# Performance work log

Hardware: AMD Instinct MI355X
Metric: run time of the kernel (lower is better)

Reference implementation:

```python
import jax, jax.numpy as jnp
import numpy as np

EPS = 1e-6
SIGMA_C = 2.0
PAD = 0
VOCAB = 100
D_EMB = 384


def setup_inputs() -> dict:
    key = jax.random.key(0)
    k1, k2, k3 = jax.random.split(key, 3)
    B, L = 32, 1025  # L odd so durs[:,1::2] and durs[:,2::2] align
    text = jax.random.randint(k1, (B, L), 0, VOCAB)
    durs = jax.random.randint(k2, (B, L), 0, 4)
    emb_table = jax.random.normal(k3, (VOCAB, D_EMB), dtype=jnp.float32)
    return {"text": text, "durs": durs, "emb_table": emb_table, "total_time": 2048}


def reference(text, durs, emb_table, total_time):
    # --- merge blank/token pairs (as in GaussianEmbedding.forward) ---
    text_m = jnp.concatenate([text[:, :1], text[:, 1::2]], axis=1)              # [B,N]
    durs_m = jnp.concatenate([durs[:, :1], durs[:, 1::2] + durs[:, 2::2]], axis=1)  # [B,N]
    embed = emb_table[text_m]                                                    # [B,N,E]

    # --- Gaussian length regulation ---
    d = durs_m.astype(jnp.float32)
    cum = jnp.cumsum(d, axis=-1)                 # [B,N] end times
    c = cum - 0.5 * d                            # [B,N] token centers
    sig = d / SIGMA_C + EPS                      # [B,N]
    t = jnp.arange(total_time, dtype=jnp.float32) + 0.5  # [T] frame midpoints

    # Normal pdf weights [B,T,N]
    z = (t[None, :, None] - c[:, None, :]) / sig[:, None, :]
    w = jnp.exp(-0.5 * z * z) / (sig[:, None, :] * jnp.sqrt(2.0 * jnp.pi))
    # zero weight for pad tokens, normalize over tokens
    w = jnp.where((text_m == PAD)[:, None, :], 0.0, w)
    w = w / (w.sum(-1, keepdims=True) + EPS)
    # zero frames beyond each sample's total duration
    valid = t[None, :] < cum[:, -1:]             # [B,T]
    w = jnp.where(valid[..., None], w, 0.0)

    return jnp.einsum('btn,bne->bte', w, embed)  # [B,T,E]
```

## Files before the change

### kernel.cpp

```cpp
#include <hip/hip_runtime.h>
#include <hip/hip_bf16.h>

#define BATCH 32
#define LSEQ 1025
#define TT 2048
#define NTOK 513
#define EMB 384
#define FT 32
#define WMAX 120
#define INV_SQRT_2PI 0.3989422804014327f

__device__ inline float* scan513(float* src, float* dst) {
  for (int off = 1; off < NTOK; off <<= 1) {
    for (int i = threadIdx.x; i < NTOK; i += 256) {
      float v = src[i];
      if (i >= off) v += src[i - off];
      dst[i] = v;
    }
    __syncthreads();
    float* t = src; src = dst; dst = t;
  }
  return src;
}

__global__ __launch_bounds__(256) void prep_kernel(
    const int* __restrict__ text, const int* __restrict__ durs,
    float2* __restrict__ kept, int* __restrict__ counts,
    float* __restrict__ totals) {
  const int b = blockIdx.x;
  const int tid = threadIdx.x;
  __shared__ float s_a[NTOK], s_b[NTOK];
  __shared__ float s_c[NTOK];
  __shared__ float s_d[NTOK];
  __shared__ int s_tok[NTOK];

  const int* tb = text + b * LSEQ;
  const int* db = durs + b * LSEQ;
  for (int n = tid; n < NTOK; n += 256) {
    int dm, tk;
    if (n == 0) { dm = db[0]; tk = tb[0]; }
    else { dm = db[2 * n - 1] + db[2 * n]; tk = tb[2 * n - 1]; }
    s_d[n] = (float)dm;
    s_a[n] = (float)dm;
    s_tok[n] = tk;
  }
  __syncthreads();
  float* cum = scan513(s_a, s_b);
  for (int n = tid; n < NTOK; n += 256) {
    s_c[n] = cum[n] - 0.5f * s_d[n];
  }
  if (tid == 0) totals[b] = cum[NTOK - 1];
  __syncthreads();
  float* flagbuf = (cum == s_a) ? s_a : s_b;
  float* other = (cum == s_a) ? s_b : s_a;
  for (int n = tid; n < NTOK; n += 256) {
    flagbuf[n] = (s_d[n] >= 1.0f && s_tok[n] != 0) ? 1.0f : 0.0f;
  }
  __syncthreads();
  float* incl = scan513(flagbuf, other);
  for (int n = tid; n < NTOK; n += 256) {
    float d = s_d[n];
    int tk = s_tok[n];
    if (d >= 1.0f && tk != 0) {
      int pos = (int)incl[n] - 1;
      int packed = ((int)d << 17) | (tk * EMB);
      kept[b * NTOK + pos] = make_float2(s_c[n], __int_as_float(packed));
    }
  }
  if (tid == 0) counts[b] = (int)incl[NTOK - 1];
}

__global__ __launch_bounds__(192) void frames_kernel(
    const float2* __restrict__ kept, const int* __restrict__ counts,
    const float* __restrict__ totals, const float* __restrict__ emb,
    float* __restrict__ out) {
  const int t0 = blockIdx.x * FT;
  const int b = blockIdx.y;
  const int tid = threadIdx.x;

  __shared__ float4 s_tk[WMAX];
  __shared__ float s_reach[WMAX];
  __shared__ float s_w[WMAX * FT];
  __shared__ float s_factor[FT];

  const int M = counts[b];
  const float total = totals[b];
  const float2* kb = kept + b * NTOK;

  const float loB = (float)t0 - 39.5f;
  const float hiB = (float)t0 + (float)(FT - 1) + 40.5f;
  int l = 0, r = M;
  while (l < r) { int m = (l + r) >> 1; if (kb[m].x < loB) l = m + 1; else r = m; }
  const int lo = l;
  r = M;
  while (l < r) { int m = (l + r) >> 1; if (kb[m].x <= hiB) l = m + 1; else r = m; }
  int win = l - lo;
  if (win > WMAX) win = WMAX;

  for (int i = tid; i < win; i += 192) {
    float2 kv = kb[lo + i];
    int packed = __float_as_int(kv.y);
    int d = packed >> 17;
    int off = packed & 0x1FFFF;
    float df = (float)d;
    float inv_sig = 1.0f / (0.5f * df + 1e-6f);
    s_tk[i] = make_float4(kv.x, inv_sig, INV_SQRT_2PI * inv_sig,
                          __int_as_float(off));
    s_reach[i] = 6.7f * df + 1e-4f;
  }
  __syncthreads();

  const float t0f = (float)t0 + 0.5f;
  const int pairs = win * FT;
  for (int idx = tid; idx < pairs; idx += 192) {
    const int n = idx >> 5, f = idx & (FT - 1);
    const float4 tk = s_tk[n];
    const float z = (t0f + (float)f - tk.x) * tk.y;
    s_w[idx] = tk.z * __expf(-0.5f * z * z);
  }
  __syncthreads();

  if (tid < FT) {
    float s = 0.f;
    for (int n = 0; n < win; ++n) s += s_w[n * FT + tid];
    const float tf = t0f + (float)tid;
    s_factor[tid] = (tf < total) ? 1.0f / (s + 1e-6f) : 0.0f;
  }
  __syncthreads();

  const int fh = tid / 96;
  const int cg = (tid % 96) * 4;
  const int fbase = fh * 16;
  float4 acc[16];
#pragma unroll
  for (int k = 0; k < 16; ++k) acc[k] = make_float4(0.f, 0.f, 0.f, 0.f);

  const float fLo = (float)(t0 + fbase) + 0.5f;
  const float fHi = fLo + 15.0f;
  for (int n = 0; n < win; ++n) {
    const float4 tk = s_tk[n];
    const float reach = s_reach[n];
    if (tk.x + reach < fLo || tk.x - reach > fHi) continue;
    const int off = __float_as_int(tk.w);
    const float4 v = *(const float4*)(emb + off + cg);
    const float4* wp = (const float4*)(s_w + n * FT + fbase);
#pragma unroll
    for (int q = 0; q < 4; ++q) {
      const float4 w4 = wp[q];
      float4& a0 = acc[4 * q + 0];
      a0.x += w4.x * v.x; a0.y += w4.x * v.y; a0.z += w4.x * v.z; a0.w += w4.x * v.w;
      float4& a1 = acc[4 * q + 1];
      a1.x += w4.y * v.x; a1.y += w4.y * v.y; a1.z += w4.y * v.z; a1.w += w4.y * v.w;
      float4& a2 = acc[4 * q + 2];
      a2.x += w4.z * v.x; a2.y += w4.z * v.y; a2.z += w4.z * v.z; a2.w += w4.z * v.w;
      float4& a3 = acc[4 * q + 3];
      a3.x += w4.w * v.x; a3.y += w4.w * v.y; a3.z += w4.w * v.z; a3.w += w4.w * v.w;
    }
  }

  const size_t obase = ((size_t)b * TT + t0 + fbase) * EMB + cg;
#pragma unroll
  for (int k = 0; k < 16; ++k) {
    const float fac = s_factor[fbase + k];
    float4 r;
    r.x = acc[k].x * fac; r.y = acc[k].y * fac;
    r.z = acc[k].z * fac; r.w = acc[k].w * fac;
    *(float4*)(out + obase + (size_t)k * EMB) = r;
  }
}

extern "C" void kernel_launch(void* const* d_in, const int* in_sizes, int n_in,
                              void* d_out, int out_size, void* d_ws,
                              size_t ws_size, hipStream_t stream) {
  const int* text = (const int*)d_in[0];
  const int* durs = (const int*)d_in[1];
  const float* emb = (const float*)d_in[2];
  float* out = (float*)d_out;

  float2* kept = (float2*)d_ws;
  int* counts = (int*)(kept + BATCH * NTOK);
  float* totals = (float*)(counts + BATCH);

  prep_kernel<<<BATCH, 256, 0, stream>>>(text, durs, kept, counts, totals);
  frames_kernel<<<dim3(TT / FT, BATCH), 192, 0, stream>>>(kept, counts, totals,
                                                          emb, out);
}
```

Measured before the change: 133.5 us.

## Compute Gaussian weights in registers per frame and shrink frame tile to 16

The frames kernel now uses 16-frame tiles. Each thread owns one frame and a 32-float slice of the embedding row, and computes its own Gaussian weight and weight sum in registers. This drops the shared weight buffer, the separate normalization pass and two barriers. Tiles starting past the sample's total duration skip all work. In exchange every thread recomputes exp per token, the embedding reads are less coalesced (each thread reads 8 consecutive float4s), and twice as many blocks run.

```diff
diff --git a/kernel.cpp b/kernel.cpp
--- a/kernel.cpp
+++ b/kernel.cpp
@@ -6,8 +6,8 @@
 #define TT 2048
 #define NTOK 513
 #define EMB 384
-#define FT 32
-#define WMAX 120
+#define FT 16
+#define WMAX 104
 #define INV_SQRT_2PI 0.3989422804014327f
 
 __device__ inline float* scan513(float* src, float* dst) {
@@ -77,18 +77,18 @@
   const int t0 = blockIdx.x * FT;
   const int b = blockIdx.y;
   const int tid = threadIdx.x;
+  const int f = tid & 15;
+  const int q = tid >> 4;
 
   __shared__ float4 s_tk[WMAX];
   __shared__ float s_reach[WMAX];
-  __shared__ float s_w[WMAX * FT];
-  __shared__ float s_factor[FT];
 
   const int M = counts[b];
   const float total = totals[b];
   const float2* kb = kept + b * NTOK;
 
-  const float loB = (float)t0 - 39.5f;
-  const float hiB = (float)t0 + (float)(FT - 1) + 40.5f;
+  const float loB = (float)t0 - 40.5f;
+  const float hiB = (float)t0 + 56.0f;
   int l = 0, r = M;
   while (l < r) { int m = (l + r) >> 1; if (kb[m].x < loB) l = m + 1; else r = m; }
   const int lo = l;
@@ -96,6 +96,7 @@
   while (l < r) { int m = (l + r) >> 1; if (kb[m].x <= hiB) l = m + 1; else r = m; }
   int win = l - lo;
   if (win > WMAX) win = WMAX;
+  if ((float)t0 + 0.5f >= total) win = 0;
 
   for (int i = tid; i < win; i += 192) {
     float2 kv = kb[lo + i];
@@ -110,62 +111,40 @@
   }
   __syncthreads();
 
-  const float t0f = (float)t0 + 0.5f;
-  const int pairs = win * FT;
-  for (int idx = tid; idx < pairs; idx += 192) {
-    const int n = idx >> 5, f = idx & (FT - 1);
-    const float4 tk = s_tk[n];
-    const float z = (t0f + (float)f - tk.x) * tk.y;
-    s_w[idx] = tk.z * __expf(-0.5f * z * z);
-  }
-  __syncthreads();
+  const float tf = (float)t0 + (float)f + 0.5f;
+  const float tileLo = (float)t0 + 0.5f;
+  const float tileHi = (float)t0 + 15.5f;
 
-  if (tid < FT) {
-    float s = 0.f;
-    for (int n = 0; n < win; ++n) s += s_w[n * FT + tid];
-    const float tf = t0f + (float)tid;
-    s_factor[tid] = (tf < total) ? 1.0f / (s + 1e-6f) : 0.0f;
-  }
-  __syncthreads();
+  float wsum = 0.f;
+  float4 acc[8];
+#pragma unroll
+  for (int j = 0; j < 8; ++j) acc[j] = make_float4(0.f, 0.f, 0.f, 0.f);
 
-  const int fh = tid / 96;
-  const int cg = (tid % 96) * 4;
-  const int fbase = fh * 16;
-  float4 acc[16];
-#pragma unroll
-  for (int k = 0; k < 16; ++k) acc[k] = make_float4(0.f, 0.f, 0.f, 0.f);
-
-  const float fLo = (float)(t0 + fbase) + 0.5f;
-  const float fHi = fLo + 15.0f;
   for (int n = 0; n < win; ++n) {
     const float4 tk = s_tk[n];
     const float reach = s_reach[n];
-    if (tk.x + reach < fLo || tk.x - reach > fHi) continue;
-    const int off = __float_as_int(tk.w);
-    const float4 v = *(const float4*)(emb + off + cg);
-    const float4* wp = (const float4*)(s_w + n * FT + fbase);
+    if (tk.x + reach < tileLo || tk.x - reach > tileHi) continue;
+    const float z = (tf - tk.x) * tk.y;
+    const float w = tk.z * __expf(-0.5f * z * z);
+    wsum += w;
+    const float4* vrow = (const float4*)(emb + (__float_as_int(tk.w) & 0x1FFFF))
+                         + q * 8;
 #pragma unroll
-    for (int q = 0; q < 4; ++q) {
-      const float4 w4 = wp[q];
-      float4& a0 = acc[4 * q + 0];
-      a0.x += w4.x * v.x; a0.y += w4.x * v.y; a0.z += w4.x * v.z; a0.w += w4.x * v.w;
-      float4& a1 = acc[4 * q + 1];
-      a1.x += w4.y * v.x; a1.y += w4.y * v.y; a1.z += w4.y * v.z; a1.w += w4.y * v.w;
-      float4& a2 = acc[4 * q + 2];
-      a2.x += w4.z * v.x; a2.y += w4.z * v.y; a2.z += w4.z * v.z; a2.w += w4.z * v.w;
-      float4& a3 = acc[4 * q + 3];
-      a3.x += w4.w * v.x; a3.y += w4.w * v.y; a3.z += w4.w * v.z; a3.w += w4.w * v.w;
+    for (int j = 0; j < 8; ++j) {
+      const float4 v = vrow[j];
+      acc[j].x += w * v.x; acc[j].y += w * v.y;
+      acc[j].z += w * v.z; acc[j].w += w * v.w;
     }
   }
 
-  const size_t obase = ((size_t)b * TT + t0 + fbase) * EMB + cg;
+  const float fac = (tf < total) ? 1.0f / (wsum + 1e-6f) : 0.0f;
+  float4* orow = (float4*)(out + ((size_t)b * TT + t0 + f) * EMB) + q * 8;
 #pragma unroll
-  for (int k = 0; k < 16; ++k) {
-    const float fac = s_factor[fbase + k];
-    float4 r;
-    r.x = acc[k].x * fac; r.y = acc[k].y * fac;
-    r.z = acc[k].z * fac; r.w = acc[k].w * fac;
-    *(float4*)(out + obase + (size_t)k * EMB) = r;
+  for (int j = 0; j < 8; ++j) {
+    float4 rv;
+    rv.x = acc[j].x * fac; rv.y = acc[j].y * fac;
+    rv.z = acc[j].z * fac; rv.w = acc[j].w * fac;
+    orow[j] = rv;
   }
 }
 
```

Result: slower. 172.1 us (+28.9%).
